# Performance work log

Measured on AMD Instinct MI355X. Metric: run time of the kernel, lower is better.

## Reference

```python
import jax, jax.numpy as jnp
import numpy as np

B, N, D, H = 4, 2048, 768, 12
HD = D // H
SCALE = HD ** -0.5


def setup_inputs() -> dict:
    key = jax.random.key(0)
    k1, k2, k3 = jax.random.split(key, 3)
    x = jax.random.normal(k1, (B, N, D), dtype=jnp.float32)
    w_qkv = jax.random.normal(k2, (D, 3 * D), dtype=jnp.float32) * (D ** -0.5)
    w_proj = jax.random.normal(k3, (D, D), dtype=jnp.float32) * (D ** -0.5)
    b_proj = jnp.zeros((D,), dtype=jnp.float32)
    return {"x": x, "w_qkv": w_qkv, "w_proj": w_proj, "b_proj": b_proj}


def reference(x, w_qkv, w_proj, b_proj):
    b, n, d = x.shape
    qkv = x @ w_qkv                      # [b, n, 3d]
    q, k, v = jnp.split(qkv, 3, axis=-1)
    # [b, n, d] -> [b, h, n, hd]
    split_heads = lambda t: t.reshape(b, n, H, HD).transpose(0, 2, 1, 3)
    q, k, v = split_heads(q), split_heads(k), split_heads(v)
    dots = jnp.einsum('bhqd,bhkd->bhqk', q, k) * SCALE   # [b, h, n, n]
    attn = jax.nn.softmax(dots, axis=-1)
    q_attn = attn[:, :, 0, :]            # attention row of query token 0: [b, h, n]
    # dropout p=0 (eval) -> identity
    out = jnp.einsum('bhqk,bhkd->bhqd', attn, v)          # [b, h, n, hd]
    out = out.transpose(0, 2, 1, 3).reshape(b, n, d)      # [b, n, d]
    return out @ w_proj + b_proj, q_attn
```

## Files before the change

kernel.cpp:

```cpp
#include <hip/hip_runtime.h>


typedef unsigned short u16;
typedef __attribute__((ext_vector_type(8))) short bf8;
typedef __attribute__((ext_vector_type(4))) short bf4;
typedef __attribute__((ext_vector_type(4))) float f4;

#define MFMA16(a, b, c) __builtin_amdgcn_mfma_f32_16x16x32_bf16((a), (b), (c), 0, 0, 0)

#if __has_builtin(__builtin_amdgcn_exp2f)
#define EXP2(x) __builtin_amdgcn_exp2f(x)
#else
#define EXP2(x) __expf((x) * 0.6931471805599453f)
#endif

__device__ __forceinline__ float b2f(u16 h) {
  union { unsigned u; float f; } v; v.u = ((unsigned)h) << 16; return v.f;
}
__device__ __forceinline__ u16 f2b(float f) {
  union { float f; unsigned u; } v; v.f = f;
  unsigned r = v.u + 0x7fffu + ((v.u >> 16) & 1u);
  return (u16)(r >> 16);
}
__device__ __forceinline__ u16 f2bt(float f) {
  union { float f; unsigned u; } v; v.f = f;
  return (u16)(v.u >> 16);
}
__device__ __forceinline__ void gload16(const u16* g, u16* l) {
  __builtin_amdgcn_global_load_lds(
      (const __attribute__((address_space(1))) void*)g,
      (__attribute__((address_space(3))) void*)l, 16, 0, 0);
}

__global__ __launch_bounds__(256) void detect_dtype(
    const u16* __restrict__ x, unsigned* __restrict__ flag) {
  __shared__ int any;
  if (threadIdx.x == 0) any = 0;
  __syncthreads();
  unsigned b = x[2 * threadIdx.x];
  unsigned e = (b >> 7) & 0xFF;
  if (e >= 0x8E) atomicOr(&any, 1);
  __syncthreads();
  if (threadIdx.x == 0) *flag = (unsigned)(any ? 1 : 0);
}

__global__ __launch_bounds__(256) void convert_bf16(
    const void* __restrict__ in, u16* __restrict__ out, int n,
    const unsigned* __restrict__ flag) {
  const int f32 = (int)*flag;
  for (int i = blockIdx.x * 256 + threadIdx.x; i < n; i += gridDim.x * 256)
    out[i] = f32 ? f2b(((const float*)in)[i]) : ((const u16*)in)[i];
}

__global__ __launch_bounds__(256) void transpose_any(
    const void* __restrict__ in, u16* __restrict__ out, int R, int C,
    const unsigned* __restrict__ flag) {
  __shared__ u16 tile[32][33];
  const int f32 = (int)*flag;
  const int bx = blockIdx.x * 32;
  const int by = blockIdx.y * 32;
  const int tx = threadIdx.x & 31, ty = threadIdx.x >> 5;
#pragma unroll
  for (int i = 0; i < 4; i++) {
    size_t idx = (size_t)(by + ty + i * 8) * C + bx + tx;
    tile[ty + i * 8][tx] = f32 ? f2b(((const float*)in)[idx]) : ((const u16*)in)[idx];
  }
  __syncthreads();
#pragma unroll
  for (int i = 0; i < 4; i++)
    out[(size_t)(bx + ty + i * 8) * R + by + tx] = tile[tx][ty + i * 8];
}

__global__ __launch_bounds__(256) void transpose_v(
    const u16* __restrict__ qkv, u16* __restrict__ Vt) {
  __shared__ u16 tile[64][65];
  const int n0 = blockIdx.x * 64, h = blockIdx.y, b = blockIdx.z;
  {
    const int d = threadIdx.x & 63, nq = threadIdx.x >> 6;
#pragma unroll
    for (int i = 0; i < 16; i++) {
      int n = i * 4 + nq;
      tile[n][d] = qkv[(size_t)(b * 2048 + n0 + n) * 2304 + 1536 + h * 64 + d];
    }
  }
  __syncthreads();
  {
    const int n = threadIdx.x & 63, dq = threadIdx.x >> 6;
    const int n2 = (n & ~31) | (((n >> 2) & 3) << 3) | (((n >> 4) & 1) << 2) | (n & 3);
#pragma unroll
    for (int i = 0; i < 16; i++) {
      int d2 = i * 4 + dq;
      Vt[(size_t)((b * 12 + h) * 64 + d2) * 2048 + n0 + n2] = tile[n][d2];
    }
  }
}

template <int BIAS>
__global__ __launch_bounds__(256) void gemm_bt(
    const u16* __restrict__ A, const u16* __restrict__ Bt,
    const void* __restrict__ bias, void* __restrict__ C,
    int M, int Ncols, int K, const unsigned* __restrict__ outflag) {
  __shared__ alignas(16) u16 Al[2][128 * 32];
  __shared__ alignas(16) u16 Bl[2][128 * 32];
  const int t = threadIdx.x;
  const int lane = t & 63, wave = t >> 6;
  const int wr = wave >> 1, wc = wave & 1;
  const int quad = lane >> 4, l16 = lane & 15;
  const int bm = blockIdx.y * 128, bn = blockIdx.x * 128;
  const int f32o = outflag ? (int)*outflag : 0;
  const int grow = lane >> 2, gcol = (lane & 3) * 8;
  const int chunk0 = wave * 2, chunk1 = wave * 2 + 1;
  const int arow0 = chunk0 * 16 + grow, arow1 = chunk1 * 16 + grow;
  f4 acc[4][4] = {};
  gload16(A + (size_t)(bm + arow0) * K + gcol, &Al[0][chunk0 * 512]);
  gload16(Bt + (size_t)(bn + arow0) * K + gcol, &Bl[0][chunk0 * 512]);
  gload16(A + (size_t)(bm + arow1) * K + gcol, &Al[0][chunk1 * 512]);
  gload16(Bt + (size_t)(bn + arow1) * K + gcol, &Bl[0][chunk1 * 512]);
  const int NIT = K >> 5;
  for (int i = 0; i < NIT; i++) {
    const int cur = i & 1, nxt = cur ^ 1;
    __syncthreads();
    if (i + 1 < NIT) {
      int k0 = (i + 1) << 5;
      gload16(A + (size_t)(bm + arow0) * K + k0 + gcol, &Al[nxt][chunk0 * 512]);
      gload16(Bt + (size_t)(bn + arow0) * K + k0 + gcol, &Bl[nxt][chunk0 * 512]);
      gload16(A + (size_t)(bm + arow1) * K + k0 + gcol, &Al[nxt][chunk1 * 512]);
      gload16(Bt + (size_t)(bn + arow1) * K + k0 + gcol, &Bl[nxt][chunk1 * 512]);
    }
    bf8 af[4], bfr[4];
#pragma unroll
    for (int mt = 0; mt < 4; mt++)
      af[mt] = *(const bf8*)&Al[cur][(wr * 64 + mt * 16 + l16) * 32 + quad * 8];
#pragma unroll
    for (int nt = 0; nt < 4; nt++)
      bfr[nt] = *(const bf8*)&Bl[cur][(wc * 64 + nt * 16 + l16) * 32 + quad * 8];
#pragma unroll
    for (int mt = 0; mt < 4; mt++)
#pragma unroll
      for (int nt = 0; nt < 4; nt++)
        acc[mt][nt] = MFMA16(af[mt], bfr[nt], acc[mt][nt]);
  }
#pragma unroll
  for (int mt = 0; mt < 4; mt++) {
    int row = bm + wr * 64 + mt * 16 + quad * 4;
#pragma unroll
    for (int nt = 0; nt < 4; nt++) {
      int col = bn + wc * 64 + nt * 16 + l16;
      float bv = 0.f;
      if (BIAS)
        bv = f32o ? ((const float*)bias)[col] : b2f(((const u16*)bias)[col]);
#pragma unroll
      for (int r = 0; r < 4; r++) {
        size_t idx = (size_t)(row + r) * Ncols + col;
        float v = acc[mt][nt][r] + bv;
        if (f32o) ((float*)C)[idx] = v; else ((u16*)C)[idx] = f2b(v);
      }
    }
  }
}

__global__ __launch_bounds__(256, 3) void flash_attn(
    const u16* __restrict__ qkv, const u16* __restrict__ Vt,
    u16* __restrict__ O, float* __restrict__ qe, float* __restrict__ lout) {
  const int STR = 72;
  __shared__ alignas(16) u16 Kl[64 * 72];
  __shared__ alignas(16) u16 Vl[64 * 72];
  const int t = threadIdx.x, lane = t & 63, wave = t >> 6;
  const int quad = lane >> 4, l16 = lane & 15;
  const int id = blockIdx.x;
  const int bh = (id & 7) + 8 * (id >> 7);
  const int qtile = (id >> 3) & 15;
  const int b = bh / 12, h = bh - b * 12;
  const int q0 = qtile * 128 + wave * 32;
  const bool dumpP = (qe != nullptr) && (qtile == 0) && (wave == 0);
  const float SCALE2 = 0.125f * 1.44269504089f;
  const float M0 = 16.f;
  bf8 qf[2][2];
#pragma unroll
  for (int qt = 0; qt < 2; qt++) {
    const u16* Qr = qkv + (size_t)(b * 2048 + q0 + qt * 16 + l16) * 2304 + h * 64;
    bf8 r0 = *(const bf8*)(Qr + quad * 8);
    bf8 r1 = *(const bf8*)(Qr + 32 + quad * 8);
#pragma unroll
    for (int j = 0; j < 8; j++) {
      qf[qt][0][j] = (short)f2b(b2f((u16)r0[j]) * SCALE2);
      qf[qt][1][j] = (short)f2b(b2f((u16)r1[j]) * SCALE2);
    }
  }
  const u16* Kb = qkv + (size_t)(b * 2048) * 2304 + 768 + h * 64;
  const u16* Vb = Vt + (size_t)((b * 12 + h) * 64) * 2048;
  const int srow = t >> 3, sc8 = (t & 7) * 8;
  const int srow2 = srow + 32;
  f4 o[2][4] = {};
  float lpart[2] = {0.f, 0.f};

  bf8 kreg0 = *(const bf8*)(Kb + (size_t)srow * 2304 + sc8);
  bf8 kreg1 = *(const bf8*)(Kb + (size_t)srow2 * 2304 + sc8);
  bf8 vreg0 = *(const bf8*)(Vb + (size_t)srow * 2048 + sc8);
  bf8 vreg1 = *(const bf8*)(Vb + (size_t)srow2 * 2048 + sc8);

  for (int i = 0; i < 32; i++) {
    __syncthreads();
    *(bf8*)&Kl[srow * STR + sc8] = kreg0;
    *(bf8*)&Kl[srow2 * STR + sc8] = kreg1;
    *(bf8*)&Vl[srow * STR + sc8] = vreg0;
    *(bf8*)&Vl[srow2 * STR + sc8] = vreg1;
    __syncthreads();
    if (i < 31) {
      const u16* Kn = Kb + (size_t)(i * 64 + 64) * 2304;
      const u16* Vn = Vb + (i * 64 + 64);
      kreg0 = *(const bf8*)(Kn + (size_t)srow * 2304 + sc8);
      kreg1 = *(const bf8*)(Kn + (size_t)srow2 * 2304 + sc8);
      vreg0 = *(const bf8*)(Vn + (size_t)srow * 2048 + sc8);
      vreg1 = *(const bf8*)(Vn + (size_t)srow2 * 2048 + sc8);
    }
    bf8 pf[2][2];
#pragma unroll
    for (int kt = 0; kt < 4; kt++) {
      bf8 kf0 = *(const bf8*)&Kl[(kt * 16 + l16) * STR + quad * 8];
      bf8 kf1 = *(const bf8*)&Kl[(kt * 16 + l16) * STR + 32 + quad * 8];
#pragma unroll
      for (int qt = 0; qt < 2; qt++) {
        f4 z = {};
        z = MFMA16(kf0, qf[qt][0], z);
        z = MFMA16(kf1, qf[qt][1], z);
        float e0 = EXP2(z[0] - M0);
        float e1 = EXP2(z[1] - M0);
        float e2 = EXP2(z[2] - M0);
        float e3 = EXP2(z[3] - M0);
        lpart[qt] += (e0 + e1) + (e2 + e3);
        if (qt == 0 && dumpP && l16 == 0) {
          f4 ev = {e0, e1, e2, e3};
          *(f4*)&qe[bh * 2048 + i * 64 + kt * 16 + quad * 4] = ev;
        }
        pf[qt][kt >> 1][(kt & 1) * 4 + 0] = (short)f2bt(e0);
        pf[qt][kt >> 1][(kt & 1) * 4 + 1] = (short)f2bt(e1);
        pf[qt][kt >> 1][(kt & 1) * 4 + 2] = (short)f2bt(e2);
        pf[qt][kt >> 1][(kt & 1) * 4 + 3] = (short)f2bt(e3);
      }
    }
#pragma unroll
    for (int pair = 0; pair < 2; pair++) {
#pragma unroll
      for (int nt = 0; nt < 4; nt++) {
        bf8 vf = *(const bf8*)&Vl[(nt * 16 + l16) * STR + pair * 32 + quad * 8];
        o[0][nt] = MFMA16(vf, pf[0][pair], o[0][nt]);
        o[1][nt] = MFMA16(vf, pf[1][pair], o[1][nt]);
      }
    }
  }
#pragma unroll
  for (int qt = 0; qt < 2; qt++) {
    float l = lpart[qt];
    l += __shfl_xor(l, 16, 64);
    l += __shfl_xor(l, 32, 64);
    if (qt == 0 && dumpP && lane == 0) lout[bh] = l;
    float inv = 1.f / l;
    size_t row = (size_t)(b * 2048 + q0 + qt * 16 + l16) * 768 + h * 64;
#pragma unroll
    for (int nt = 0; nt < 4; nt++) {
      bf4 pk = {(short)f2b(o[qt][nt][0] * inv), (short)f2b(o[qt][nt][1] * inv),
                (short)f2b(o[qt][nt][2] * inv), (short)f2b(o[qt][nt][3] * inv)};
      *(bf4*)&O[row + nt * 16 + quad * 4] = pk;
    }
  }
}

__global__ __launch_bounds__(256) void qattn_norm(
    const float* __restrict__ qe, const float* __restrict__ lout,
    void* __restrict__ out, const unsigned* __restrict__ flag) {
  const int bh = blockIdx.x;
  const int f32o = (int)*flag;
  const float inv = 1.f / lout[bh];
  for (int k = threadIdx.x; k < 2048; k += 256) {
    size_t idx = (size_t)6291456 + (size_t)bh * 2048 + k;
    float v = qe[bh * 2048 + k] * inv;
    if (f32o) ((float*)out)[idx] = v; else ((u16*)out)[idx] = f2b(v);
  }
}

__global__ __launch_bounds__(256) void qattn_row0(
    const u16* __restrict__ qkv, void* __restrict__ out,
    const unsigned* __restrict__ flag) {
  const int bh = blockIdx.x, b = bh / 12, h = bh % 12;
  __shared__ float qs[64];
  __shared__ float sv[2048];
  __shared__ float red[8];
  const int t = threadIdx.x;
  const int f32o = (int)*flag;
  if (t < 64) qs[t] = b2f(qkv[(size_t)(b * 2048) * 2304 + h * 64 + t]);
  __syncthreads();
  float lmax = -1e30f;
  for (int k = t; k < 2048; k += 256) {
    const u16* Kr = qkv + (size_t)(b * 2048 + k) * 2304 + 768 + h * 64;
    float acc = 0.f;
#pragma unroll
    for (int j = 0; j < 8; j++) {
      bf8 kv = *(const bf8*)(Kr + j * 8);
#pragma unroll
      for (int d = 0; d < 8; d++) acc += qs[j * 8 + d] * b2f((u16)kv[d]);
    }
    acc *= 0.125f;
    sv[k] = acc;
    lmax = fmaxf(lmax, acc);
  }
#pragma unroll
  for (int off = 32; off >= 1; off >>= 1) lmax = fmaxf(lmax, __shfl_xor(lmax, off, 64));
  if ((t & 63) == 0) red[t >> 6] = lmax;
  __syncthreads();
  const float bmax = fmaxf(fmaxf(red[0], red[1]), fmaxf(red[2], red[3]));
  float lsum = 0.f;
  for (int k = t; k < 2048; k += 256) {
    float e = __expf(sv[k] - bmax);
    sv[k] = e;
    lsum += e;
  }
#pragma unroll
  for (int off = 32; off >= 1; off >>= 1) lsum += __shfl_xor(lsum, off, 64);
  if ((t & 63) == 0) red[4 + (t >> 6)] = lsum;
  __syncthreads();
  const float inv = 1.f / (red[4] + red[5] + red[6] + red[7]);
  for (int k = t; k < 2048; k += 256) {
    size_t idx = (size_t)6291456 + (size_t)bh * 2048 + k;
    float v = sv[k] * inv;
    if (f32o) ((float*)out)[idx] = v; else ((u16*)out)[idx] = f2b(v);
  }
}

extern "C" void kernel_launch(void* const* d_in, const int* in_sizes, int n_in,
                              void* d_out, int out_size, void* d_ws, size_t ws_size,
                              hipStream_t stream) {
  const void* x_raw      = d_in[0];
  const void* w_qkv_raw  = d_in[1];
  const void* w_proj_raw = d_in[2];
  const void* b_proj_raw = d_in[3];
  char* ws = (char*)d_ws;
  unsigned* flag = (unsigned*)ws;
  u16* xbf    = (u16*)(ws + 256);
  u16* wqkvT  = (u16*)(ws + 12583168);
  u16* wprojT = (u16*)(ws + 16122112);
  u16* qkv    = (u16*)(ws + 17301760);
  u16* Vt     = (u16*)(ws + 55050496);
  float* qe   = (float*)(ws + 67633408);
  float* lout = (float*)(ws + 68026624);
  u16* attn   = xbf;
  const bool fused = ws_size >= 68026816ull;

  detect_dtype<<<1, 256, 0, stream>>>((const u16*)x_raw, flag);
  convert_bf16<<<2048, 256, 0, stream>>>(x_raw, xbf, 6291456, flag);
  transpose_any<<<dim3(2304 / 32, 768 / 32), 256, 0, stream>>>(w_qkv_raw, wqkvT, 768, 2304, flag);
  transpose_any<<<dim3(768 / 32, 768 / 32), 256, 0, stream>>>(w_proj_raw, wprojT, 768, 768, flag);
  gemm_bt<0><<<dim3(2304 / 128, 8192 / 128), 256, 0, stream>>>(
      xbf, wqkvT, nullptr, qkv, 8192, 2304, 768, nullptr);
  transpose_v<<<dim3(2048 / 64, 12, 4), 256, 0, stream>>>(qkv, Vt);
  flash_attn<<<dim3(768), 256, 0, stream>>>(qkv, Vt, attn,
                                            fused ? qe : nullptr,
                                            fused ? lout : nullptr);
  if (fused)
    qattn_norm<<<dim3(48), 256, 0, stream>>>(qe, lout, d_out, flag);
  else
    qattn_row0<<<dim3(48), 256, 0, stream>>>(qkv, d_out, flag);
  gemm_bt<1><<<dim3(768 / 128, 8192 / 128), 256, 0, stream>>>(
      attn, wprojT, b_proj_raw, d_out, 8192, 768, 768, flag);
}
```

Before: 239.2 us.

## Fuse V transpose into QKV GEMM, inline dtype detect, double-buffer attention K/V

Several changes land together. The dtype-detect kernel is replaced by an inline wave ballot in each consumer, and the two weight transposes are merged into one launch. The QKV GEMM now writes the V columns directly in the transposed, permuted layout, so the separate transpose_v pass is dropped. The flash attention loop double-buffers K/V in LDS, which removes one barrier per iteration, and the max offset is folded into the MFMA accumulator init. These aim to cut launch count, global round trips and sync overhead, at the cost of more LDS in attention and redundant per-block detection reads.

```diff
diff --git a/kernel.cpp b/kernel.cpp
--- a/kernel.cpp
+++ b/kernel.cpp
@@ -31,32 +31,30 @@
       (const __attribute__((address_space(1))) void*)g,
       (__attribute__((address_space(3))) void*)l, 16, 0, 0);
 }
-
-__global__ __launch_bounds__(256) void detect_dtype(
-    const u16* __restrict__ x, unsigned* __restrict__ flag) {
-  __shared__ int any;
-  if (threadIdx.x == 0) any = 0;
-  __syncthreads();
-  unsigned b = x[2 * threadIdx.x];
-  unsigned e = (b >> 7) & 0xFF;
-  if (e >= 0x8E) atomicOr(&any, 1);
-  __syncthreads();
-  if (threadIdx.x == 0) *flag = (unsigned)(any ? 1 : 0);
+__device__ __forceinline__ int detect_f32(const u16* x) {
+  unsigned v = x[2 * (threadIdx.x & 63)];
+  unsigned e = (v >> 7) & 0xFF;
+  return __ballot(e >= 0x8E) != 0ull;
 }
 
 __global__ __launch_bounds__(256) void convert_bf16(
-    const void* __restrict__ in, u16* __restrict__ out, int n,
-    const unsigned* __restrict__ flag) {
-  const int f32 = (int)*flag;
+    const void* __restrict__ in, u16* __restrict__ out, int n) {
+  const int f32 = detect_f32((const u16*)in);
   for (int i = blockIdx.x * 256 + threadIdx.x; i < n; i += gridDim.x * 256)
     out[i] = f32 ? f2b(((const float*)in)[i]) : ((const u16*)in)[i];
 }
 
-__global__ __launch_bounds__(256) void transpose_any(
-    const void* __restrict__ in, u16* __restrict__ out, int R, int C,
-    const unsigned* __restrict__ flag) {
+__global__ __launch_bounds__(256) void transpose_two(
+    const void* __restrict__ wqkv, u16* __restrict__ wqkvT,
+    const void* __restrict__ wproj, u16* __restrict__ wprojT,
+    const u16* __restrict__ xdet) {
+  const int z = blockIdx.z;
+  if (z == 1 && blockIdx.x >= 24) return;
+  const void* in = z ? wproj : wqkv;
+  u16* out = z ? wprojT : wqkvT;
+  const int R = 768, C = z ? 768 : 2304;
   __shared__ u16 tile[32][33];
-  const int f32 = (int)*flag;
+  const int f32 = detect_f32(xdet);
   const int bx = blockIdx.x * 32;
   const int by = blockIdx.y * 32;
   const int tx = threadIdx.x & 31, ty = threadIdx.x >> 5;
@@ -71,35 +69,12 @@
     out[(size_t)(bx + ty + i * 8) * R + by + tx] = tile[tx][ty + i * 8];
 }
 
-__global__ __launch_bounds__(256) void transpose_v(
-    const u16* __restrict__ qkv, u16* __restrict__ Vt) {
-  __shared__ u16 tile[64][65];
-  const int n0 = blockIdx.x * 64, h = blockIdx.y, b = blockIdx.z;
-  {
-    const int d = threadIdx.x & 63, nq = threadIdx.x >> 6;
-#pragma unroll
-    for (int i = 0; i < 16; i++) {
-      int n = i * 4 + nq;
-      tile[n][d] = qkv[(size_t)(b * 2048 + n0 + n) * 2304 + 1536 + h * 64 + d];
-    }
-  }
-  __syncthreads();
-  {
-    const int n = threadIdx.x & 63, dq = threadIdx.x >> 6;
-    const int n2 = (n & ~31) | (((n >> 2) & 3) << 3) | (((n >> 4) & 1) << 2) | (n & 3);
-#pragma unroll
-    for (int i = 0; i < 16; i++) {
-      int d2 = i * 4 + dq;
-      Vt[(size_t)((b * 12 + h) * 64 + d2) * 2048 + n0 + n2] = tile[n][d2];
-    }
-  }
-}
-
 template <int BIAS>
-__global__ __launch_bounds__(256) void gemm_bt(
+__global__ __launch_bounds__(256, 4) void gemm_bt(
     const u16* __restrict__ A, const u16* __restrict__ Bt,
     const void* __restrict__ bias, void* __restrict__ C,
-    int M, int Ncols, int K, const unsigned* __restrict__ outflag) {
+    int M, int Ncols, int K, const u16* __restrict__ xdet,
+    u16* __restrict__ Vt) {
   __shared__ alignas(16) u16 Al[2][128 * 32];
   __shared__ alignas(16) u16 Bl[2][128 * 32];
   const int t = threadIdx.x;
@@ -107,7 +82,7 @@
   const int wr = wave >> 1, wc = wave & 1;
   const int quad = lane >> 4, l16 = lane & 15;
   const int bm = blockIdx.y * 128, bn = blockIdx.x * 128;
-  const int f32o = outflag ? (int)*outflag : 0;
+  const int f32o = BIAS ? detect_f32(xdet) : 0;
   const int grow = lane >> 2, gcol = (lane & 3) * 8;
   const int chunk0 = wave * 2, chunk1 = wave * 2 + 1;
   const int arow0 = chunk0 * 16 + grow, arow1 = chunk1 * 16 + grow;
@@ -140,6 +115,23 @@
       for (int nt = 0; nt < 4; nt++)
         acc[mt][nt] = MFMA16(af[mt], bfr[nt], acc[mt][nt]);
   }
+  if (Vt != nullptr && bn >= 1536) {
+    const int b = bm >> 11;
+#pragma unroll
+    for (int mt = 0; mt < 4; mt++) {
+      int n0 = (bm & 2047) + wr * 64 + mt * 16 + quad * 4;
+      int n2 = (n0 & ~31) | (((n0 >> 2) & 3) << 3) | (((n0 >> 4) & 1) << 2);
+#pragma unroll
+      for (int nt = 0; nt < 4; nt++) {
+        int colv = bn - 1536 + wc * 64 + nt * 16 + l16;
+        int h = colv >> 6, d = colv & 63;
+        bf4 pk = {(short)f2b(acc[mt][nt][0]), (short)f2b(acc[mt][nt][1]),
+                  (short)f2b(acc[mt][nt][2]), (short)f2b(acc[mt][nt][3])};
+        *(bf4*)&Vt[(size_t)((b * 12 + h) * 64 + d) * 2048 + n2] = pk;
+      }
+    }
+    return;
+  }
 #pragma unroll
   for (int mt = 0; mt < 4; mt++) {
     int row = bm + wr * 64 + mt * 16 + quad * 4;
@@ -163,8 +155,8 @@
     const u16* __restrict__ qkv, const u16* __restrict__ Vt,
     u16* __restrict__ O, float* __restrict__ qe, float* __restrict__ lout) {
   const int STR = 72;
-  __shared__ alignas(16) u16 Kl[64 * 72];
-  __shared__ alignas(16) u16 Vl[64 * 72];
+  __shared__ alignas(16) u16 Kl[2][64 * 72];
+  __shared__ alignas(16) u16 Vl[2][64 * 72];
   const int t = threadIdx.x, lane = t & 63, wave = t >> 6;
   const int quad = lane >> 4, l16 = lane & 15;
   const int id = blockIdx.x;
@@ -174,7 +166,7 @@
   const int q0 = qtile * 128 + wave * 32;
   const bool dumpP = (qe != nullptr) && (qtile == 0) && (wave == 0);
   const float SCALE2 = 0.125f * 1.44269504089f;
-  const float M0 = 16.f;
+  const float mM0 = -16.f;
   bf8 qf[2][2];
 #pragma unroll
   for (int qt = 0; qt < 2; qt++) {
@@ -198,36 +190,36 @@
   bf8 kreg1 = *(const bf8*)(Kb + (size_t)srow2 * 2304 + sc8);
   bf8 vreg0 = *(const bf8*)(Vb + (size_t)srow * 2048 + sc8);
   bf8 vreg1 = *(const bf8*)(Vb + (size_t)srow2 * 2048 + sc8);
+  *(bf8*)&Kl[0][srow * STR + sc8] = kreg0;
+  *(bf8*)&Kl[0][srow2 * STR + sc8] = kreg1;
+  *(bf8*)&Vl[0][srow * STR + sc8] = vreg0;
+  *(bf8*)&Vl[0][srow2 * STR + sc8] = vreg1;
+  {
+    const u16* Kn = Kb + (size_t)64 * 2304;
+    const u16* Vn = Vb + 64;
+    kreg0 = *(const bf8*)(Kn + (size_t)srow * 2304 + sc8);
+    kreg1 = *(const bf8*)(Kn + (size_t)srow2 * 2304 + sc8);
+    vreg0 = *(const bf8*)(Vn + (size_t)srow * 2048 + sc8);
+    vreg1 = *(const bf8*)(Vn + (size_t)srow2 * 2048 + sc8);
+  }
 
   for (int i = 0; i < 32; i++) {
+    const int cur = i & 1, nxt = cur ^ 1;
     __syncthreads();
-    *(bf8*)&Kl[srow * STR + sc8] = kreg0;
-    *(bf8*)&Kl[srow2 * STR + sc8] = kreg1;
-    *(bf8*)&Vl[srow * STR + sc8] = vreg0;
-    *(bf8*)&Vl[srow2 * STR + sc8] = vreg1;
-    __syncthreads();
-    if (i < 31) {
-      const u16* Kn = Kb + (size_t)(i * 64 + 64) * 2304;
-      const u16* Vn = Vb + (i * 64 + 64);
-      kreg0 = *(const bf8*)(Kn + (size_t)srow * 2304 + sc8);
-      kreg1 = *(const bf8*)(Kn + (size_t)srow2 * 2304 + sc8);
-      vreg0 = *(const bf8*)(Vn + (size_t)srow * 2048 + sc8);
-      vreg1 = *(const bf8*)(Vn + (size_t)srow2 * 2048 + sc8);
-    }
     bf8 pf[2][2];
 #pragma unroll
     for (int kt = 0; kt < 4; kt++) {
-      bf8 kf0 = *(const bf8*)&Kl[(kt * 16 + l16) * STR + quad * 8];
-      bf8 kf1 = *(const bf8*)&Kl[(kt * 16 + l16) * STR + 32 + quad * 8];
+      bf8 kf0 = *(const bf8*)&Kl[cur][(kt * 16 + l16) * STR + quad * 8];
+      bf8 kf1 = *(const bf8*)&Kl[cur][(kt * 16 + l16) * STR + 32 + quad * 8];
 #pragma unroll
       for (int qt = 0; qt < 2; qt++) {
-        f4 z = {};
+        f4 z = {mM0, mM0, mM0, mM0};
         z = MFMA16(kf0, qf[qt][0], z);
         z = MFMA16(kf1, qf[qt][1], z);
-        float e0 = EXP2(z[0] - M0);
-        float e1 = EXP2(z[1] - M0);
-        float e2 = EXP2(z[2] - M0);
-        float e3 = EXP2(z[3] - M0);
+        float e0 = EXP2(z[0]);
+        float e1 = EXP2(z[1]);
+        float e2 = EXP2(z[2]);
+        float e3 = EXP2(z[3]);
         lpart[qt] += (e0 + e1) + (e2 + e3);
         if (qt == 0 && dumpP && l16 == 0) {
           f4 ev = {e0, e1, e2, e3};
@@ -243,10 +235,24 @@
     for (int pair = 0; pair < 2; pair++) {
 #pragma unroll
       for (int nt = 0; nt < 4; nt++) {
-        bf8 vf = *(const bf8*)&Vl[(nt * 16 + l16) * STR + pair * 32 + quad * 8];
+        bf8 vf = *(const bf8*)&Vl[cur][(nt * 16 + l16) * STR + pair * 32 + quad * 8];
         o[0][nt] = MFMA16(vf, pf[0][pair], o[0][nt]);
         o[1][nt] = MFMA16(vf, pf[1][pair], o[1][nt]);
       }
+    }
+    if (i + 1 < 32) {
+      *(bf8*)&Kl[nxt][srow * STR + sc8] = kreg0;
+      *(bf8*)&Kl[nxt][srow2 * STR + sc8] = kreg1;
+      *(bf8*)&Vl[nxt][srow * STR + sc8] = vreg0;
+      *(bf8*)&Vl[nxt][srow2 * STR + sc8] = vreg1;
+    }
+    if (i + 2 < 32) {
+      const u16* Kn = Kb + (size_t)(i * 64 + 128) * 2304;
+      const u16* Vn = Vb + (i * 64 + 128);
+      kreg0 = *(const bf8*)(Kn + (size_t)srow * 2304 + sc8);
+      kreg1 = *(const bf8*)(Kn + (size_t)srow2 * 2304 + sc8);
+      vreg0 = *(const bf8*)(Vn + (size_t)srow * 2048 + sc8);
+      vreg1 = *(const bf8*)(Vn + (size_t)srow2 * 2048 + sc8);
     }
   }
 #pragma unroll
@@ -268,9 +274,9 @@
 
 __global__ __launch_bounds__(256) void qattn_norm(
     const float* __restrict__ qe, const float* __restrict__ lout,
-    void* __restrict__ out, const unsigned* __restrict__ flag) {
+    void* __restrict__ out, const u16* __restrict__ xdet) {
   const int bh = blockIdx.x;
-  const int f32o = (int)*flag;
+  const int f32o = detect_f32(xdet);
   const float inv = 1.f / lout[bh];
   for (int k = threadIdx.x; k < 2048; k += 256) {
     size_t idx = (size_t)6291456 + (size_t)bh * 2048 + k;
@@ -281,13 +287,13 @@
 
 __global__ __launch_bounds__(256) void qattn_row0(
     const u16* __restrict__ qkv, void* __restrict__ out,
-    const unsigned* __restrict__ flag) {
+    const u16* __restrict__ xdet) {
   const int bh = blockIdx.x, b = bh / 12, h = bh % 12;
   __shared__ float qs[64];
   __shared__ float sv[2048];
   __shared__ float red[8];
   const int t = threadIdx.x;
-  const int f32o = (int)*flag;
+  const int f32o = detect_f32(xdet);
   if (t < 64) qs[t] = b2f(qkv[(size_t)(b * 2048) * 2304 + h * 64 + t]);
   __syncthreads();
   float lmax = -1e30f;
@@ -334,8 +340,8 @@
   const void* w_qkv_raw  = d_in[1];
   const void* w_proj_raw = d_in[2];
   const void* b_proj_raw = d_in[3];
+  const u16* xdet = (const u16*)x_raw;
   char* ws = (char*)d_ws;
-  unsigned* flag = (unsigned*)ws;
   u16* xbf    = (u16*)(ws + 256);
   u16* wqkvT  = (u16*)(ws + 12583168);
   u16* wprojT = (u16*)(ws + 16122112);
@@ -346,20 +352,18 @@
   u16* attn   = xbf;
   const bool fused = ws_size >= 68026816ull;
 
-  detect_dtype<<<1, 256, 0, stream>>>((const u16*)x_raw, flag);
-  convert_bf16<<<2048, 256, 0, stream>>>(x_raw, xbf, 6291456, flag);
-  transpose_any<<<dim3(2304 / 32, 768 / 32), 256, 0, stream>>>(w_qkv_raw, wqkvT, 768, 2304, flag);
-  transpose_any<<<dim3(768 / 32, 768 / 32), 256, 0, stream>>>(w_proj_raw, wprojT, 768, 768, flag);
-  gemm_bt<0><<<dim3(2304 / 128, 8192 / 128), 256, 0, stream>>>(
-      xbf, wqkvT, nullptr, qkv, 8192, 2304, 768, nullptr);
-  transpose_v<<<dim3(2048 / 64, 12, 4), 256, 0, stream>>>(qkv, Vt);
+  convert_bf16<<<2048, 256, 0, stream>>>(x_raw, xbf, 6291456);
+  transpose_two<<<dim3(72, 24, 2), 256, 0, stream>>>(
+      w_qkv_raw, wqkvT, w_proj_raw, wprojT, xdet);
+  gemm_bt<0><<<dim3(18, 64), 256, 0, stream>>>(
+      xbf, wqkvT, nullptr, qkv, 8192, 2304, 768, xdet, Vt);
   flash_attn<<<dim3(768), 256, 0, stream>>>(qkv, Vt, attn,
                                             fused ? qe : nullptr,
                                             fused ? lout : nullptr);
   if (fused)
-    qattn_norm<<<dim3(48), 256, 0, stream>>>(qe, lout, d_out, flag);
+    qattn_norm<<<dim3(48), 256, 0, stream>>>(qe, lout, d_out, xdet);
   else
-    qattn_row0<<<dim3(48), 256, 0, stream>>>(qkv, d_out, flag);
-  gemm_bt<1><<<dim3(768 / 128, 8192 / 128), 256, 0, stream>>>(
-      attn, wprojT, b_proj_raw, d_out, 8192, 768, 768, flag);
-}
+    qattn_row0<<<dim3(48), 256, 0, stream>>>(qkv, d_out, xdet);
+  gemm_bt<1><<<dim3(6, 64), 256, 0, stream>>>(
+      attn, wprojT, b_proj_raw, d_out, 8192, 768, 768, xdet, nullptr);
+}
```

Result: faster. 227.9 us (-4.7%).
